# Kernel optimization log

Measured on AMD Instinct MI355X. Metric: run time of the kernel, lower is better.

The kernel has to match this reference:

```python
import jax, jax.numpy as jnp
import numpy as np

B, L, E, H = 64, 512, 128, 256


def setup_inputs() -> dict:
    key = jax.random.key(0)
    ks = jax.random.split(key, 16)
    s = 0.05
    return {
        "embedded_inputs": jax.random.normal(ks[0], (B, L, E), jnp.float32),
        "decoder_input": jax.random.normal(ks[1], (B, E), jnp.float32),
        "h0": jax.random.normal(ks[2], (B, H), jnp.float32),
        "c0": jax.random.normal(ks[3], (B, H), jnp.float32),
        "context": jax.random.normal(ks[4], (B, L, H), jnp.float32),
        # LSTM cell params
        "Wi": jax.random.normal(ks[5], (4 * H, E), jnp.float32) * s,
        "bi": jnp.zeros((4 * H,), jnp.float32),
        "Wh": jax.random.normal(ks[6], (4 * H, H), jnp.float32) * s,
        "bh": jnp.zeros((4 * H,), jnp.float32),
        # hidden_out: Linear(2H -> H)
        "Wo": jax.random.normal(ks[7], (H, 2 * H), jnp.float32) * s,
        "bo": jnp.zeros((H,), jnp.float32),
        # attention params: input_linear(H->H), context conv1d(H->H,k=1), V [H]
        "Wa_in": jax.random.normal(ks[8], (H, H), jnp.float32) * s,
        "ba_in": jnp.zeros((H,), jnp.float32),
        "Wa_ctx": jax.random.normal(ks[9], (H, H), jnp.float32) * s,
        "ba_ctx": jnp.zeros((H,), jnp.float32),
        "V": jax.random.normal(ks[10], (H,), jnp.float32) * s,
    }


def reference(embedded_inputs, decoder_input, h0, c0, context,
              Wi, bi, Wh, bh, Wo, bo, Wa_in, ba_in, Wa_ctx, ba_ctx, V):
    # Precompute projected context once (Conv1d with kernel 1 == per-position linear): [B,L,H]
    ctx_proj = jnp.einsum('blh,gh->blg', context, Wa_ctx) + ba_ctx

    def step(carry, _):
        dec_in, h, c, mask = carry
        gates = dec_in @ Wi.T + bi + h @ Wh.T + bh              # [B,4H]
        i_g, f_g, g_g, o_g = jnp.split(gates, 4, axis=1)
        i_g = jax.nn.sigmoid(i_g)
        f_g = jax.nn.sigmoid(f_g)
        g_g = jnp.tanh(g_g)
        o_g = jax.nn.sigmoid(o_g)
        c_t = f_g * c + i_g * g_g
        h_t = o_g * jnp.tanh(c_t)
        # attention
        inp = h_t @ Wa_in.T + ba_in                              # [B,H]
        scores = jnp.einsum('h,blh->bl', V, jnp.tanh(inp[:, None, :] + ctx_proj))
        scores = jnp.where(mask == 0, -jnp.inf, scores)
        alpha = jax.nn.softmax(scores, axis=1)                   # [B,L]
        att_hidden = jnp.einsum('bl,blh->bh', alpha, ctx_proj)
        hidden_t = jnp.tanh(jnp.concatenate([att_hidden, h_t], axis=1) @ Wo.T + bo)
        # pointer: argmax over still-available positions
        masked_outs = alpha * mask
        idx = jnp.argmax(masked_outs, axis=1)                    # [B]
        one_hot = jax.nn.one_hot(idx, L, dtype=mask.dtype)
        mask_next = mask * (1.0 - one_hot)
        dec_next = jnp.take_along_axis(embedded_inputs, idx[:, None, None], axis=1)[:, 0]
        return (dec_next, hidden_t, c_t, mask_next), (alpha, idx)

    mask0 = jnp.ones((B, L), jnp.float32)
    carry0 = (decoder_input, h0, c0, mask0)
    (dec_f, h_f, c_f, _), (alphas, ptrs) = jax.lax.scan(step, carry0, None, length=L)
    outputs = jnp.transpose(alphas, (1, 0, 2))                   # [B,L,L]
    pointers = jnp.transpose(ptrs, (1, 0))                       # [B,L]
    return outputs, pointers, h_f, c_f
```

## Files before the change

kernel.cpp:

```cpp
#include <hip/hip_runtime.h>
#include <math.h>

#define SCOPE __HIP_MEMORY_SCOPE_AGENT

constexpr int Bn = 64, Ln = 512, En = 128, Hn = 256, Tn = 512;
constexpr int NBLK = 256, NTHR = 512;
constexpr int CTX_LD = 260, XPAD = 384, UPAD = 520;

constexpr int OFF_CTX = 0;
constexpr int OFF_SCR = 128 * CTX_LD;
constexpr int OFF_INP = OFF_SCR + 4096;
constexpr int OFF_SS  = OFF_INP + 256;
constexpr int OFF_ES  = OFF_SS + 128;
constexpr int OFF_MK  = OFF_ES + 128;
constexpr int OFF_VS  = OFF_MK + 128;
constexpr int OFF_GS  = OFF_VS + 256;
constexpr int OFF_ST  = OFF_GS + 256;
constexpr int OFF_WR  = OFF_ST + 64;
constexpr int OFF_BA  = OFF_WR + 64;
constexpr int OFF_HTL = OFF_BA + 256;
constexpr int SMEM_FL = OFF_HTL + 64;

constexpr size_t PTR_OFF = (size_t)Bn * Ln * Ln;
constexpr size_t HF_OFF  = PTR_OFF + (size_t)Bn * Ln;
constexpr size_t CF_OFF  = HF_OFF + (size_t)Bn * Hn;

constexpr int GQ_HT    = 0;
constexpr int GQ_HID   = 1024;
constexpr int GQ_ATT   = 2048;
constexpr int GQ_STATS = 6144;
constexpr int GQ_INPP  = 6208;
constexpr int GQ_STRIDE = 6208 + 16384;

__device__ __forceinline__ float fast_tanh(float x) {
  const float e = __expf(2.0f * x);
  return 1.0f - __fdividef(2.0f, 1.0f + e);
}
__device__ __forceinline__ float sigmoidf_(float x) {
  return 1.0f / (1.0f + expf(-x));
}
__device__ __forceinline__ void llc_storef(float* p, float v) {
  __hip_atomic_store(p, v, __ATOMIC_RELAXED, SCOPE);
}
__device__ __forceinline__ float4 llc_ld4(const float* p) {
  float4 r;
  asm volatile("global_load_dwordx4 %0, %1, off sc0 sc1\n\ts_waitcnt vmcnt(0)"
               : "=&v"(r) : "v"(p) : "memory");
  return r;
}
__device__ __forceinline__ void llc_ld4x4(const float* p0, const float* p1,
                                          const float* p2, const float* p3,
                                          float4& a, float4& b, float4& c, float4& d) {
  asm volatile(
      "global_load_dwordx4 %0, %4, off sc0 sc1\n\t"
      "global_load_dwordx4 %1, %5, off sc0 sc1\n\t"
      "global_load_dwordx4 %2, %6, off sc0 sc1\n\t"
      "global_load_dwordx4 %3, %7, off sc0 sc1\n\t"
      "s_waitcnt vmcnt(0)"
      : "=&v"(a), "=&v"(b), "=&v"(c), "=&v"(d)
      : "v"(p0), "v"(p1), "v"(p2), "v"(p3) : "memory");
}
__device__ __forceinline__ void llc_ld5(const float* p0, const float* p1,
                                        const float* p2, const float* p3,
                                        const float* p4,
                                        float4& a, float4& b, float4& c,
                                        float4& d, float4& e) {
  asm volatile(
      "global_load_dwordx4 %0, %5, off sc0 sc1\n\t"
      "global_load_dwordx4 %1, %6, off sc0 sc1\n\t"
      "global_load_dwordx4 %2, %7, off sc0 sc1\n\t"
      "global_load_dwordx4 %3, %8, off sc0 sc1\n\t"
      "global_load_dwordx4 %4, %9, off sc0 sc1\n\t"
      "s_waitcnt vmcnt(0)"
      : "=&v"(a), "=&v"(b), "=&v"(c), "=&v"(d), "=&v"(e)
      : "v"(p0), "v"(p1), "v"(p2), "v"(p3), "v"(p4) : "memory");
}

__device__ __forceinline__ void group_barrier16(unsigned* flags_g, int j, unsigned tgt) {
  asm volatile("s_waitcnt vmcnt(0)" ::: "memory");
  __syncthreads();
  if (threadIdx.x == 0)
    __hip_atomic_store(&flags_g[j * 32], tgt, __ATOMIC_RELAXED, SCOPE);
  if (threadIdx.x < 16) {
    long spins = 0;
    while (__hip_atomic_load(&flags_g[threadIdx.x * 32], __ATOMIC_RELAXED, SCOPE) < tgt) {
      __builtin_amdgcn_s_sleep(1);
      if (++spins > 50000000L) __builtin_trap();
    }
  }
  __syncthreads();
  asm volatile("" ::: "memory");
}

#define DOT4(acc, w4, x4) \
  acc = fmaf((w4).x, (x4).x, fmaf((w4).y, (x4).y, fmaf((w4).z, (x4).z, fmaf((w4).w, (x4).w, (acc)))))

__global__ void __launch_bounds__(NTHR, 1)
decoder_main(const float* __restrict__ emb, const float* __restrict__ dec0,
             const float* __restrict__ h0,  const float* __restrict__ c0,
             const float* __restrict__ ctxg,const float* __restrict__ Wi,
             const float* __restrict__ bi,  const float* __restrict__ Wh,
             const float* __restrict__ bh,  const float* __restrict__ Wo,
             const float* __restrict__ bo,  const float* __restrict__ Wain,
             const float* __restrict__ bain,const float* __restrict__ Wactx,
             const float* __restrict__ bactx,const float* __restrict__ Vv,
             float* __restrict__ out, unsigned* __restrict__ flags,
             float* __restrict__ wsd)
{
  extern __shared__ float sm[];
  float* ctx    = sm + OFF_CTX;
  float* scr    = sm + OFF_SCR;
  float* x_s    = sm + OFF_SCR;
  float* inp_s  = sm + OFF_INP;
  float* s_s    = sm + OFF_SS;
  float* e_s    = sm + OFF_ES;
  float* mask_s = sm + OFF_MK;
  float* V_s    = sm + OFF_VS;
  float* gsum   = sm + OFF_GS;
  float* stats_s= sm + OFF_ST;
  float* wred   = sm + OFF_WR;
  float* bain_s = sm + OFF_BA;
  float* htl_s  = sm + OFF_HTL;
  int*   wredi  = (int*)wred;

  const int tid = threadIdx.x, bid = blockIdx.x;
  const int gq = bid >> 4, j = bid & 15;
  const int bbj = j >> 2, ck = j & 3;
  const int b_ctx = gq * 4 + bbj;
  const int l0 = ck * 128;

  const int team = tid >> 3, seg8 = tid & 7;
  const int gteam = team >> 4, hloc = team & 15;
  const int r_abs = gteam * 256 + j * 16 + hloc;
  const int g2 = tid >> 1, half = tid & 1;
  const int r16loc = tid >> 5, seg32 = tid & 31;
  const int r16 = j * 16 + r16loc;
  const int hq = tid & 63, lg = tid >> 6;

  unsigned* flags_g = flags + gq * (16 * 32);
  float* wsg = wsd + (size_t)gq * GQ_STRIDE;

  float4 wg4[12];
  #pragma unroll
  for (int k = 0; k < 4; ++k) wg4[k] = *(const float4*)&Wi[(size_t)r_abs * En + k * 32 + seg8 * 4];
  #pragma unroll
  for (int k = 0; k < 8; ++k) wg4[4 + k] = *(const float4*)&Wh[(size_t)r_abs * Hn + k * 32 + seg8 * 4];
  const float bias_g = bi[r_abs] + bh[r_abs];

  float4 wa4[2];
  #pragma unroll
  for (int k = 0; k < 2; ++k)
    wa4[k] = *(const float4*)&Wain[(size_t)g2 * Hn + j * 16 + half * 8 + k * 4];

  float4 wo4[4];
  #pragma unroll
  for (int k = 0; k < 4; ++k) wo4[k] = *(const float4*)&Wo[(size_t)r16 * (2 * Hn) + k * 128 + seg32 * 4];
  const float bo_r = bo[r16];

  float cst = 0.0f;
  if (tid < 64) cst = c0[(size_t)(gq * 4 + (tid >> 4)) * Hn + j * 16 + (tid & 15)];

  if (tid < 128) mask_s[tid] = 1.0f;
  if (tid < 256) { V_s[tid] = Vv[tid]; bain_s[tid] = bain[tid]; }

  {
    const int gc = tid & 31, lgi = tid >> 5;
    float acc[8][8];
    #pragma unroll
    for (int a2 = 0; a2 < 8; ++a2)
      #pragma unroll
      for (int b2 = 0; b2 < 8; ++b2) acc[a2][b2] = 0.0f;
    float* stg_c = scr;
    float* stg_w = scr + 1024;
    for (int kc = 0; kc < 32; ++kc) {
      __syncthreads();
      for (int i = tid; i < 1024; i += NTHR) {
        int k = i & 7, l = i >> 3;
        stg_c[k * 128 + l] = ctxg[((size_t)(b_ctx * Ln + l0 + l)) * Hn + kc * 8 + k];
      }
      for (int i = tid; i < 2048; i += NTHR) {
        int k = i & 7, gg = i >> 3;
        stg_w[k * 256 + gg] = Wactx[(size_t)gg * Hn + kc * 8 + k];
      }
      __syncthreads();
      #pragma unroll
      for (int kk = 0; kk < 8; ++kk) {
        float cl[8], wgt[8];
        #pragma unroll
        for (int jj = 0; jj < 8; ++jj) cl[jj] = stg_c[kk * 128 + lgi * 8 + jj];
        #pragma unroll
        for (int jj = 0; jj < 8; ++jj) wgt[jj] = stg_w[kk * 256 + gc * 8 + jj];
        #pragma unroll
        for (int li = 0; li < 8; ++li)
          #pragma unroll
          for (int gi = 0; gi < 8; ++gi)
            acc[li][gi] = fmaf(cl[li], wgt[gi], acc[li][gi]);
      }
    }
    __syncthreads();
    #pragma unroll
    for (int li = 0; li < 8; ++li)
      #pragma unroll
      for (int gi = 0; gi < 8; ++gi)
        ctx[(lgi * 8 + li) * CTX_LD + gc * 8 + gi] = acc[li][gi] + bactx[gc * 8 + gi];
  }
  __syncthreads();

  unsigned tgt = 1;
  int w0 = 0, w1 = 0, w2 = 0, w3 = 0;

  for (int t = 0; t < Tn; ++t) {
    {
      if (tid < 256) {
        const int bbx = tid >> 6, h4 = tid & 63;
        float4 v;
        if (t == 0) v = *(const float4*)&h0[(size_t)(gq * 4 + bbx) * Hn + h4 * 4];
        else        v = llc_ld4(wsg + GQ_HID + bbx * 256 + h4 * 4);
        *(float4*)&x_s[bbx * XPAD + 128 + h4 * 4] = v;
      } else if (tid < 384) {
        const int i2 = tid - 256, bbx = i2 >> 5, k4 = i2 & 31;
        const int gb = gq * 4 + bbx;
        float4 v;
        if (t == 0) v = *(const float4*)&dec0[(size_t)gb * En + k4 * 4];
        else {
          const int wsel = (bbx == 0) ? w0 : (bbx == 1) ? w1 : (bbx == 2) ? w2 : w3;
          v = *(const float4*)&emb[((size_t)gb * Ln + wsel) * En + k4 * 4];
        }
        *(float4*)&x_s[bbx * XPAD + k4 * 4] = v;
      }
      __syncthreads();
      #pragma unroll
      for (int bb = 0; bb < 4; ++bb) {
        float acc = 0.0f;
        #pragma unroll
        for (int k = 0; k < 12; ++k) {
          const float4 x4 = *(const float4*)&x_s[bb * XPAD + k * 32 + seg8 * 4];
          DOT4(acc, wg4[k], x4);
        }
        acc += __shfl_xor(acc, 1, 64);
        acc += __shfl_xor(acc, 2, 64);
        acc += __shfl_xor(acc, 4, 64);
        if (seg8 == 0) gsum[bb * 64 + team] = acc + bias_g;
      }
      __syncthreads();
      if (tid < 64) {
        const int bbx = tid >> 4, hx = tid & 15;
        const float iv = gsum[bbx * 64 + hx];
        const float fv = gsum[bbx * 64 + 16 + hx];
        const float gv = gsum[bbx * 64 + 32 + hx];
        const float ov = gsum[bbx * 64 + 48 + hx];
        const float cn = sigmoidf_(fv) * cst + sigmoidf_(iv) * tanhf(gv);
        const float htv = sigmoidf_(ov) * tanhf(cn);
        cst = cn;
        htl_s[bbx * 16 + hx] = htv;
        llc_storef(wsg + GQ_HT + bbx * 256 + j * 16 + hx, htv);
        if (t == Tn - 1) out[CF_OFF + (size_t)(gq * 4 + bbx) * Hn + j * 16 + hx] = cn;
      }
      __syncthreads();
      {
        float pac[4];
        #pragma unroll
        for (int bb = 0; bb < 4; ++bb) {
          float acc = 0.0f;
          #pragma unroll
          for (int k = 0; k < 2; ++k) {
            const float4 x4 = *(const float4*)&htl_s[bb * 16 + half * 8 + k * 4];
            DOT4(acc, wa4[k], x4);
          }
          pac[bb] = acc;
        }
        #pragma unroll
        for (int bb = 0; bb < 4; ++bb) {
          const float o = __shfl_xor(pac[bb], 1, 64);
          pac[bb] += o;
        }
        if (half == 0) {
          #pragma unroll
          for (int bb = 0; bb < 4; ++bb)
            llc_storef(wsg + GQ_INPP + bb * 4096 + g2 * 16 + j, pac[bb]);
        }
      }
    }
    group_barrier16(flags_g, j, tgt++);

    {
      if (tid < 256) {
        const float* ib = wsg + GQ_INPP + bbj * 4096 + tid * 16;
        float4 a0, a1, a2, a3;
        llc_ld4x4(ib, ib + 4, ib + 8, ib + 12, a0, a1, a2, a3);
        const float s01 = ((a0.x + a0.y) + (a0.z + a0.w)) + ((a1.x + a1.y) + (a1.z + a1.w));
        const float s23 = ((a2.x + a2.y) + (a2.z + a2.w)) + ((a3.x + a3.y) + (a3.z + a3.w));
        inp_s[tid] = s01 + s23 + bain_s[tid];
      }
      __syncthreads();
      const float4 in4 = *(const float4*)&inp_s[hq * 4];
      const float4 v4  = *(const float4*)&V_s[hq * 4];
      float4 c4[16];
      #pragma unroll
      for (int li = 0; li < 16; ++li)
        c4[li] = *(const float4*)&ctx[(lg * 16 + li) * CTX_LD + hq * 4];
      #pragma unroll
      for (int li = 0; li < 16; ++li) {
        float p;
        p = v4.x * fast_tanh(in4.x + c4[li].x);
        p = fmaf(v4.y, fast_tanh(in4.y + c4[li].y), p);
        p = fmaf(v4.z, fast_tanh(in4.z + c4[li].z), p);
        p = fmaf(v4.w, fast_tanh(in4.w + c4[li].w), p);
        p += __shfl_xor(p, 1, 64);
        p += __shfl_xor(p, 2, 64);
        p += __shfl_xor(p, 4, 64);
        p += __shfl_xor(p, 8, 64);
        p += __shfl_xor(p, 16, 64);
        p += __shfl_xor(p, 32, 64);
        if (hq == 0) {
          const int l = lg * 16 + li;
          s_s[l] = (mask_s[l] == 0.0f) ? -INFINITY : p;
        }
      }
      __syncthreads();
      if (tid < 128) {
        const float sv = s_s[tid];
        const float e = expf(sv);
        e_s[tid] = e;
        float ssum = e;
        #pragma unroll
        for (int m = 1; m < 64; m <<= 1) ssum += __shfl_xor(ssum, m, 64);
        float cv = sv; int ci = tid;
        #pragma unroll
        for (int m = 1; m < 64; m <<= 1) {
          const float ov = __shfl_xor(cv, m, 64);
          const int   oi = __shfl_xor(ci, m, 64);
          if (ov > cv || (ov == cv && oi < ci)) { cv = ov; ci = oi; }
        }
        if ((tid & 63) == 0) {
          wred[tid >> 6] = ssum;
          wred[4 + (tid >> 6)] = cv;
          wredi[8 + (tid >> 6)] = ci;
        }
      }
      __syncthreads();
      if (tid == 0) {
        const float S = wred[0] + wred[1];
        float bv = wred[4]; int bI = wredi[8];
        if (wred[5] > bv || (wred[5] == bv && wredi[9] < bI)) { bv = wred[5]; bI = wredi[9]; }
        float* stb = wsg + GQ_STATS + (bbj * 4 + ck) * 4;
        llc_storef(stb + 0, S);
        llc_storef(stb + 1, bv);
        llc_storef(stb + 2, (float)(l0 + bI));
      }
      {
        float p0 = 0, p1 = 0, p2 = 0, p3 = 0;
        #pragma unroll
        for (int li = 0; li < 16; ++li) {
          const float ev = e_s[lg * 16 + li];
          p0 = fmaf(ev, c4[li].x, p0);
          p1 = fmaf(ev, c4[li].y, p1);
          p2 = fmaf(ev, c4[li].z, p2);
          p3 = fmaf(ev, c4[li].w, p3);
        }
        *(float4*)&scr[lg * 256 + hq * 4] = make_float4(p0, p1, p2, p3);
      }
      __syncthreads();
      if (tid < 256) {
        float a = 0.0f;
        #pragma unroll
        for (int r2 = 0; r2 < 8; ++r2) a += scr[r2 * 256 + tid];
        llc_storef(wsg + GQ_ATT + (bbj * 4 + ck) * 256 + tid, a);
      }
    }
    group_barrier16(flags_g, j, tgt++);

    {
      float4 a0, a1, a2, a3, htv4;
      if (tid >= 256 && tid < 272) {
        const float4 st = llc_ld4(wsg + GQ_STATS + (tid - 256) * 4);
        *(float4*)&stats_s[(tid - 256) * 4] = st;
      }
      if (tid < 256) {
        const int bbx = tid >> 6, h4 = tid & 63;
        const float* ab = wsg + GQ_ATT + bbx * 1024 + h4 * 4;
        llc_ld5(ab, ab + 256, ab + 512, ab + 768, wsg + GQ_HT + tid * 4,
                a0, a1, a2, a3, htv4);
      }
      __syncthreads();
      float Sb[4]; int wq[4];
      #pragma unroll
      for (int bb = 0; bb < 4; ++bb) {
        Sb[bb] = ((stats_s[(bb * 4 + 0) * 4] + stats_s[(bb * 4 + 1) * 4])
                  + stats_s[(bb * 4 + 2) * 4]) + stats_s[(bb * 4 + 3) * 4];
        float bv = stats_s[(bb * 4 + 0) * 4 + 1];
        int bI = (int)stats_s[(bb * 4 + 0) * 4 + 2];
        #pragma unroll
        for (int c2 = 1; c2 < 4; ++c2) {
          const float v2 = stats_s[(bb * 4 + c2) * 4 + 1];
          const int i2 = (int)stats_s[(bb * 4 + c2) * 4 + 2];
          if (v2 > bv || (v2 == bv && i2 < bI)) { bv = v2; bI = i2; }
        }
        wq[bb] = bI;
      }
      const float Sown = (bbj == 0) ? Sb[0] : (bbj == 1) ? Sb[1] : (bbj == 2) ? Sb[2] : Sb[3];
      const int wown = (bbj == 0) ? wq[0] : (bbj == 1) ? wq[1] : (bbj == 2) ? wq[2] : wq[3];
      if (tid < 32) {
        const float4 e4 = *(const float4*)&e_s[tid * 4];
        *(float4*)&out[(size_t)b_ctx * Ln * Ln + (size_t)t * Ln + l0 + tid * 4] =
            make_float4(e4.x / Sown, e4.y / Sown, e4.z / Sown, e4.w / Sown);
      }
      if (tid == 0) {
        if (wown >= l0 && wown < l0 + 128) mask_s[wown - l0] = 0.0f;
        if (ck == 0) out[PTR_OFF + (size_t)b_ctx * Ln + t] = (float)wown;
      }
      if (tid < 256) {
        const int bbx = tid >> 6, h4 = tid & 63;
        const float Sx = (bbx == 0) ? Sb[0] : (bbx == 1) ? Sb[1] : (bbx == 2) ? Sb[2] : Sb[3];
        float4 u4;
        u4.x = (((a0.x + a1.x) + a2.x) + a3.x) / Sx;
        u4.y = (((a0.y + a1.y) + a2.y) + a3.y) / Sx;
        u4.z = (((a0.z + a1.z) + a2.z) + a3.z) / Sx;
        u4.w = (((a0.w + a1.w) + a2.w) + a3.w) / Sx;
        *(float4*)&scr[bbx * UPAD + h4 * 4] = u4;
        *(float4*)&scr[bbx * UPAD + 256 + h4 * 4] = htv4;
      }
      __syncthreads();
      #pragma unroll
      for (int bb = 0; bb < 4; ++bb) {
        float acc = 0.0f;
        #pragma unroll
        for (int k = 0; k < 4; ++k) {
          const float4 x4 = *(const float4*)&scr[bb * UPAD + k * 128 + seg32 * 4];
          DOT4(acc, wo4[k], x4);
        }
        acc += __shfl_xor(acc, 1, 64);
        acc += __shfl_xor(acc, 2, 64);
        acc += __shfl_xor(acc, 4, 64);
        acc += __shfl_xor(acc, 8, 64);
        acc += __shfl_xor(acc, 16, 64);
        if (seg32 == 0) {
          const float hv = tanhf(acc + bo_r);
          llc_storef(wsg + GQ_HID + bb * 256 + r16, hv);
          if (t == Tn - 1) out[HF_OFF + (size_t)(gq * 4 + bb) * Hn + r16] = hv;
        }
      }
      w0 = wq[0]; w1 = wq[1]; w2 = wq[2]; w3 = wq[3];
    }
    group_barrier16(flags_g, j, tgt++);
  }
}

extern "C" void kernel_launch(void* const* d_in, const int* in_sizes, int n_in,
                              void* d_out, int out_size, void* d_ws, size_t ws_size,
                              hipStream_t stream) {
  (void)in_sizes; (void)n_in; (void)out_size; (void)ws_size;
  (void)hipFuncSetAttribute(reinterpret_cast<const void*>(decoder_main),
                            hipFuncAttributeMaxDynamicSharedMemorySize, SMEM_FL * 4);
  (void)hipMemsetAsync(d_ws, 0, 32768, stream);

  const float* emb   = (const float*)d_in[0];
  const float* dec0  = (const float*)d_in[1];
  const float* h0    = (const float*)d_in[2];
  const float* c0    = (const float*)d_in[3];
  const float* ctxg  = (const float*)d_in[4];
  const float* Wi    = (const float*)d_in[5];
  const float* bi    = (const float*)d_in[6];
  const float* Wh    = (const float*)d_in[7];
  const float* bh    = (const float*)d_in[8];
  const float* Wo    = (const float*)d_in[9];
  const float* bo    = (const float*)d_in[10];
  const float* Wain  = (const float*)d_in[11];
  const float* bain  = (const float*)d_in[12];
  const float* Wactx = (const float*)d_in[13];
  const float* bactx = (const float*)d_in[14];
  const float* V     = (const float*)d_in[15];

  unsigned* flags = (unsigned*)d_ws;
  float* wsd = (float*)((char*)d_ws + 32768);

  decoder_main<<<NBLK, NTHR, SMEM_FL * 4, stream>>>(
      emb, dec0, h0, c0, ctxg, Wi, bi, Wh, bh, Wo, bo, Wain, bain, Wactx, bactx, V,
      (float*)d_out, flags, wsd);
}
```

Before: 11.49 ms.

## Split work across 512 blocks with 2 batches per 16-block group

Doubles the grid to 512 blocks so each 16-block group handles 2 batch rows instead of 4, with each block owning 64 context positions. Per-block shared memory, register arrays and per-step matvec work are halved, and launch bounds now allow 4 blocks per CU. The score reduction is rewritten as a transpose-style shuffle tree, and context values are reloaded from LDS rather than held in registers. In exchange there are twice as many groups doing barrier synchronisation and more partial stats to merge through the last-level cache.

```diff
diff --git a/kernel.cpp b/kernel.cpp
--- a/kernel.cpp
+++ b/kernel.cpp
@@ -4,33 +4,32 @@
 #define SCOPE __HIP_MEMORY_SCOPE_AGENT
 
 constexpr int Bn = 64, Ln = 512, En = 128, Hn = 256, Tn = 512;
-constexpr int NBLK = 256, NTHR = 512;
-constexpr int CTX_LD = 260, XPAD = 384, UPAD = 520;
+constexpr int NBLK = 512, NTHR = 512;
+constexpr int CTX_LD = 256, XPAD = 384, UPAD = 520;
 
 constexpr int OFF_CTX = 0;
-constexpr int OFF_SCR = 128 * CTX_LD;
-constexpr int OFF_INP = OFF_SCR + 4096;
+constexpr int OFF_SCR = 64 * CTX_LD;
+constexpr int OFF_INP = OFF_SCR + 2048;
 constexpr int OFF_SS  = OFF_INP + 256;
-constexpr int OFF_ES  = OFF_SS + 128;
-constexpr int OFF_MK  = OFF_ES + 128;
-constexpr int OFF_VS  = OFF_MK + 128;
+constexpr int OFF_ES  = OFF_SS + 64;
+constexpr int OFF_MK  = OFF_ES + 64;
+constexpr int OFF_VS  = OFF_MK + 64;
 constexpr int OFF_GS  = OFF_VS + 256;
-constexpr int OFF_ST  = OFF_GS + 256;
-constexpr int OFF_WR  = OFF_ST + 64;
-constexpr int OFF_BA  = OFF_WR + 64;
+constexpr int OFF_ST  = OFF_GS + 128;
+constexpr int OFF_BA  = OFF_ST + 64;
 constexpr int OFF_HTL = OFF_BA + 256;
-constexpr int SMEM_FL = OFF_HTL + 64;
+constexpr int SMEM_FL = OFF_HTL + 32;
 
 constexpr size_t PTR_OFF = (size_t)Bn * Ln * Ln;
 constexpr size_t HF_OFF  = PTR_OFF + (size_t)Bn * Ln;
 constexpr size_t CF_OFF  = HF_OFF + (size_t)Bn * Hn;
 
 constexpr int GQ_HT    = 0;
-constexpr int GQ_HID   = 1024;
-constexpr int GQ_ATT   = 2048;
-constexpr int GQ_STATS = 6144;
-constexpr int GQ_INPP  = 6208;
-constexpr int GQ_STRIDE = 6208 + 16384;
+constexpr int GQ_HID   = 512;
+constexpr int GQ_ATT   = 1024;
+constexpr int GQ_STATS = 5120;
+constexpr int GQ_INPP  = 5184;
+constexpr int GQ_STRIDE = 5184 + 8192;
 
 __device__ __forceinline__ float fast_tanh(float x) {
   const float e = __expf(2.0f * x);
@@ -95,7 +94,7 @@
 #define DOT4(acc, w4, x4) \
   acc = fmaf((w4).x, (x4).x, fmaf((w4).y, (x4).y, fmaf((w4).z, (x4).z, fmaf((w4).w, (x4).w, (acc)))))
 
-__global__ void __launch_bounds__(NTHR, 1)
+__global__ void __launch_bounds__(NTHR, 4)
 decoder_main(const float* __restrict__ emb, const float* __restrict__ dec0,
              const float* __restrict__ h0,  const float* __restrict__ c0,
              const float* __restrict__ ctxg,const float* __restrict__ Wi,
@@ -118,16 +117,14 @@
   float* V_s    = sm + OFF_VS;
   float* gsum   = sm + OFF_GS;
   float* stats_s= sm + OFF_ST;
-  float* wred   = sm + OFF_WR;
   float* bain_s = sm + OFF_BA;
   float* htl_s  = sm + OFF_HTL;
-  int*   wredi  = (int*)wred;
 
   const int tid = threadIdx.x, bid = blockIdx.x;
   const int gq = bid >> 4, j = bid & 15;
-  const int bbj = j >> 2, ck = j & 3;
-  const int b_ctx = gq * 4 + bbj;
-  const int l0 = ck * 128;
+  const int bbj = j >> 3, ck = j & 7;
+  const int b_ctx = gq * 2 + bbj;
+  const int l0 = ck * 64;
 
   const int team = tid >> 3, seg8 = tid & 7;
   const int gteam = team >> 4, hloc = team & 15;
@@ -158,40 +155,40 @@
   const float bo_r = bo[r16];
 
   float cst = 0.0f;
-  if (tid < 64) cst = c0[(size_t)(gq * 4 + (tid >> 4)) * Hn + j * 16 + (tid & 15)];
-
-  if (tid < 128) mask_s[tid] = 1.0f;
+  if (tid < 32) cst = c0[(size_t)(gq * 2 + (tid >> 4)) * Hn + j * 16 + (tid & 15)];
+
+  if (tid < 64) mask_s[tid] = 1.0f;
   if (tid < 256) { V_s[tid] = Vv[tid]; bain_s[tid] = bain[tid]; }
 
   {
     const int gc = tid & 31, lgi = tid >> 5;
-    float acc[8][8];
+    float acc[4][8];
     #pragma unroll
-    for (int a2 = 0; a2 < 8; ++a2)
+    for (int a2 = 0; a2 < 4; ++a2)
       #pragma unroll
       for (int b2 = 0; b2 < 8; ++b2) acc[a2][b2] = 0.0f;
     float* stg_c = scr;
-    float* stg_w = scr + 1024;
-    for (int kc = 0; kc < 32; ++kc) {
-      __syncthreads();
+    float* stg_w = scr + 256;
+    for (int kc = 0; kc < 64; ++kc) {
+      __syncthreads();
+      if (tid < 256) {
+        const int k = tid >> 6, l = tid & 63;
+        stg_c[k * 64 + l] = ctxg[((size_t)(b_ctx * Ln + l0 + l)) * Hn + kc * 4 + k];
+      }
       for (int i = tid; i < 1024; i += NTHR) {
-        int k = i & 7, l = i >> 3;
-        stg_c[k * 128 + l] = ctxg[((size_t)(b_ctx * Ln + l0 + l)) * Hn + kc * 8 + k];
-      }
-      for (int i = tid; i < 2048; i += NTHR) {
-        int k = i & 7, gg = i >> 3;
-        stg_w[k * 256 + gg] = Wactx[(size_t)gg * Hn + kc * 8 + k];
-      }
-      __syncthreads();
-      #pragma unroll
-      for (int kk = 0; kk < 8; ++kk) {
-        float cl[8], wgt[8];
-        #pragma unroll
-        for (int jj = 0; jj < 8; ++jj) cl[jj] = stg_c[kk * 128 + lgi * 8 + jj];
+        const int k = i >> 8, gg = i & 255;
+        stg_w[k * 256 + gg] = Wactx[(size_t)gg * Hn + kc * 4 + k];
+      }
+      __syncthreads();
+      #pragma unroll
+      for (int kk = 0; kk < 4; ++kk) {
+        float cl[4], wgt[8];
+        #pragma unroll
+        for (int jj = 0; jj < 4; ++jj) cl[jj] = stg_c[kk * 64 + lgi * 4 + jj];
         #pragma unroll
         for (int jj = 0; jj < 8; ++jj) wgt[jj] = stg_w[kk * 256 + gc * 8 + jj];
         #pragma unroll
-        for (int li = 0; li < 8; ++li)
+        for (int li = 0; li < 4; ++li)
           #pragma unroll
           for (int gi = 0; gi < 8; ++gi)
             acc[li][gi] = fmaf(cl[li], wgt[gi], acc[li][gi]);
@@ -199,38 +196,38 @@
     }
     __syncthreads();
     #pragma unroll
-    for (int li = 0; li < 8; ++li)
+    for (int li = 0; li < 4; ++li)
       #pragma unroll
       for (int gi = 0; gi < 8; ++gi)
-        ctx[(lgi * 8 + li) * CTX_LD + gc * 8 + gi] = acc[li][gi] + bactx[gc * 8 + gi];
+        ctx[(lgi * 4 + li) * CTX_LD + gc * 8 + gi] = acc[li][gi] + bactx[gc * 8 + gi];
   }
   __syncthreads();
 
   unsigned tgt = 1;
-  int w0 = 0, w1 = 0, w2 = 0, w3 = 0;
+  int w0 = 0, w1 = 0;
 
   for (int t = 0; t < Tn; ++t) {
     {
-      if (tid < 256) {
+      if (tid < 128) {
         const int bbx = tid >> 6, h4 = tid & 63;
         float4 v;
-        if (t == 0) v = *(const float4*)&h0[(size_t)(gq * 4 + bbx) * Hn + h4 * 4];
+        if (t == 0) v = *(const float4*)&h0[(size_t)(gq * 2 + bbx) * Hn + h4 * 4];
         else        v = llc_ld4(wsg + GQ_HID + bbx * 256 + h4 * 4);
         *(float4*)&x_s[bbx * XPAD + 128 + h4 * 4] = v;
-      } else if (tid < 384) {
-        const int i2 = tid - 256, bbx = i2 >> 5, k4 = i2 & 31;
-        const int gb = gq * 4 + bbx;
+      } else if (tid < 192) {
+        const int i2 = tid - 128, bbx = i2 >> 5, k4 = i2 & 31;
+        const int gb = gq * 2 + bbx;
         float4 v;
         if (t == 0) v = *(const float4*)&dec0[(size_t)gb * En + k4 * 4];
         else {
-          const int wsel = (bbx == 0) ? w0 : (bbx == 1) ? w1 : (bbx == 2) ? w2 : w3;
+          const int wsel = (bbx == 0) ? w0 : w1;
           v = *(const float4*)&emb[((size_t)gb * Ln + wsel) * En + k4 * 4];
         }
         *(float4*)&x_s[bbx * XPAD + k4 * 4] = v;
       }
       __syncthreads();
       #pragma unroll
-      for (int bb = 0; bb < 4; ++bb) {
+      for (int bb = 0; bb < 2; ++bb) {
         float acc = 0.0f;
         #pragma unroll
         for (int k = 0; k < 12; ++k) {
@@ -243,7 +240,7 @@
         if (seg8 == 0) gsum[bb * 64 + team] = acc + bias_g;
       }
       __syncthreads();
-      if (tid < 64) {
+      if (tid < 32) {
         const int bbx = tid >> 4, hx = tid & 15;
         const float iv = gsum[bbx * 64 + hx];
         const float fv = gsum[bbx * 64 + 16 + hx];
@@ -254,13 +251,13 @@
         cst = cn;
         htl_s[bbx * 16 + hx] = htv;
         llc_storef(wsg + GQ_HT + bbx * 256 + j * 16 + hx, htv);
-        if (t == Tn - 1) out[CF_OFF + (size_t)(gq * 4 + bbx) * Hn + j * 16 + hx] = cn;
+        if (t == Tn - 1) out[CF_OFF + (size_t)(gq * 2 + bbx) * Hn + j * 16 + hx] = cn;
       }
       __syncthreads();
       {
-        float pac[4];
-        #pragma unroll
-        for (int bb = 0; bb < 4; ++bb) {
+        float pac[2];
+        #pragma unroll
+        for (int bb = 0; bb < 2; ++bb) {
           float acc = 0.0f;
           #pragma unroll
           for (int k = 0; k < 2; ++k) {
@@ -269,15 +266,11 @@
           }
           pac[bb] = acc;
         }
-        #pragma unroll
-        for (int bb = 0; bb < 4; ++bb) {
-          const float o = __shfl_xor(pac[bb], 1, 64);
-          pac[bb] += o;
-        }
+        pac[0] += __shfl_xor(pac[0], 1, 64);
+        pac[1] += __shfl_xor(pac[1], 1, 64);
         if (half == 0) {
-          #pragma unroll
-          for (int bb = 0; bb < 4; ++bb)
-            llc_storef(wsg + GQ_INPP + bb * 4096 + g2 * 16 + j, pac[bb]);
+          llc_storef(wsg + GQ_INPP + g2 * 16 + j, pac[0]);
+          llc_storef(wsg + GQ_INPP + 4096 + g2 * 16 + j, pac[1]);
         }
       }
     }
@@ -293,32 +286,44 @@
         inp_s[tid] = s01 + s23 + bain_s[tid];
       }
       __syncthreads();
-      const float4 in4 = *(const float4*)&inp_s[hq * 4];
-      const float4 v4  = *(const float4*)&V_s[hq * 4];
-      float4 c4[16];
-      #pragma unroll
-      for (int li = 0; li < 16; ++li)
-        c4[li] = *(const float4*)&ctx[(lg * 16 + li) * CTX_LD + hq * 4];
-      #pragma unroll
-      for (int li = 0; li < 16; ++li) {
-        float p;
-        p = v4.x * fast_tanh(in4.x + c4[li].x);
-        p = fmaf(v4.y, fast_tanh(in4.y + c4[li].y), p);
-        p = fmaf(v4.z, fast_tanh(in4.z + c4[li].z), p);
-        p = fmaf(v4.w, fast_tanh(in4.w + c4[li].w), p);
-        p += __shfl_xor(p, 1, 64);
-        p += __shfl_xor(p, 2, 64);
-        p += __shfl_xor(p, 4, 64);
-        p += __shfl_xor(p, 8, 64);
-        p += __shfl_xor(p, 16, 64);
-        p += __shfl_xor(p, 32, 64);
-        if (hq == 0) {
-          const int l = lg * 16 + li;
-          s_s[l] = (mask_s[l] == 0.0f) ? -INFINITY : p;
-        }
-      }
-      __syncthreads();
-      if (tid < 128) {
+      {
+        const float4 in4 = *(const float4*)&inp_s[hq * 4];
+        const float4 v4  = *(const float4*)&V_s[hq * 4];
+        float p0, p1, p2, p3, p4, p5, p6, p7;
+        #define SCORE_P(dst, li)                                             \
+          {                                                                  \
+            const float4 c4 = *(const float4*)&ctx[(lg * 8 + (li)) * CTX_LD + hq * 4]; \
+            float p;                                                         \
+            p = v4.x * fast_tanh(in4.x + c4.x);                              \
+            p = fmaf(v4.y, fast_tanh(in4.y + c4.y), p);                      \
+            p = fmaf(v4.z, fast_tanh(in4.z + c4.z), p);                      \
+            p = fmaf(v4.w, fast_tanh(in4.w + c4.w), p);                      \
+            dst = p;                                                         \
+          }
+        SCORE_P(p0, 0) SCORE_P(p1, 1) SCORE_P(p2, 2) SCORE_P(p3, 3)
+        SCORE_P(p4, 4) SCORE_P(p5, 5) SCORE_P(p6, 6) SCORE_P(p7, 7)
+        #undef SCORE_P
+        const bool hi32 = (hq & 32) != 0;
+        float s, q0, q1, q2, q3, r0, r1, t0;
+        s = hi32 ? p0 : p4; s = __shfl_xor(s, 32, 64); q0 = (hi32 ? p4 : p0) + s;
+        s = hi32 ? p1 : p5; s = __shfl_xor(s, 32, 64); q1 = (hi32 ? p5 : p1) + s;
+        s = hi32 ? p2 : p6; s = __shfl_xor(s, 32, 64); q2 = (hi32 ? p6 : p2) + s;
+        s = hi32 ? p3 : p7; s = __shfl_xor(s, 32, 64); q3 = (hi32 ? p7 : p3) + s;
+        const bool hi16 = (hq & 16) != 0;
+        s = hi16 ? q0 : q2; s = __shfl_xor(s, 16, 64); r0 = (hi16 ? q2 : q0) + s;
+        s = hi16 ? q1 : q3; s = __shfl_xor(s, 16, 64); r1 = (hi16 ? q3 : q1) + s;
+        const bool hi8 = (hq & 8) != 0;
+        s = hi8 ? r0 : r1; s = __shfl_xor(s, 8, 64); t0 = (hi8 ? r1 : r0) + s;
+        t0 += __shfl_xor(t0, 4, 64);
+        t0 += __shfl_xor(t0, 2, 64);
+        t0 += __shfl_xor(t0, 1, 64);
+        if ((hq & 7) == 0) {
+          const int l = lg * 8 + ((hq >> 3) & 7);
+          s_s[l] = (mask_s[l] == 0.0f) ? -INFINITY : t0;
+        }
+      }
+      __syncthreads();
+      if (tid < 64) {
         const float sv = s_s[tid];
         const float e = expf(sv);
         e_s[tid] = e;
@@ -332,32 +337,26 @@
           const int   oi = __shfl_xor(ci, m, 64);
           if (ov > cv || (ov == cv && oi < ci)) { cv = ov; ci = oi; }
         }
-        if ((tid & 63) == 0) {
-          wred[tid >> 6] = ssum;
-          wred[4 + (tid >> 6)] = cv;
-          wredi[8 + (tid >> 6)] = ci;
-        }
-      }
-      __syncthreads();
-      if (tid == 0) {
-        const float S = wred[0] + wred[1];
-        float bv = wred[4]; int bI = wredi[8];
-        if (wred[5] > bv || (wred[5] == bv && wredi[9] < bI)) { bv = wred[5]; bI = wredi[9]; }
-        float* stb = wsg + GQ_STATS + (bbj * 4 + ck) * 4;
-        llc_storef(stb + 0, S);
-        llc_storef(stb + 1, bv);
-        llc_storef(stb + 2, (float)(l0 + bI));
-      }
+        if (tid == 0) {
+          float* stb = wsg + GQ_STATS + (bbj * 8 + ck) * 4;
+          llc_storef(stb + 0, ssum);
+          llc_storef(stb + 1, cv);
+          llc_storef(stb + 2, (float)(l0 + ci));
+        }
+      }
+      __syncthreads();
       {
         float p0 = 0, p1 = 0, p2 = 0, p3 = 0;
         #pragma unroll
-        for (int li = 0; li < 16; ++li) {
-          const float ev = e_s[lg * 16 + li];
-          p0 = fmaf(ev, c4[li].x, p0);
-          p1 = fmaf(ev, c4[li].y, p1);
-          p2 = fmaf(ev, c4[li].z, p2);
-          p3 = fmaf(ev, c4[li].w, p3);
-        }
+        for (int li = 0; li < 8; ++li) {
+          const float ev = e_s[lg * 8 + li];
+          const float4 c4 = *(const float4*)&ctx[(lg * 8 + li) * CTX_LD + hq * 4];
+          p0 = fmaf(ev, c4.x, p0);
+          p1 = fmaf(ev, c4.y, p1);
+          p2 = fmaf(ev, c4.z, p2);
+          p3 = fmaf(ev, c4.w, p3);
+        }
+        __syncthreads();
         *(float4*)&scr[lg * 256 + hq * 4] = make_float4(p0, p1, p2, p3);
       }
       __syncthreads();
@@ -365,64 +364,72 @@
         float a = 0.0f;
         #pragma unroll
         for (int r2 = 0; r2 < 8; ++r2) a += scr[r2 * 256 + tid];
-        llc_storef(wsg + GQ_ATT + (bbj * 4 + ck) * 256 + tid, a);
+        llc_storef(wsg + GQ_ATT + (bbj * 8 + ck) * 256 + tid, a);
       }
     }
     group_barrier16(flags_g, j, tgt++);
 
     {
-      float4 a0, a1, a2, a3, htv4;
+      float4 sum4 = make_float4(0, 0, 0, 0), htv4 = make_float4(0, 0, 0, 0);
       if (tid >= 256 && tid < 272) {
         const float4 st = llc_ld4(wsg + GQ_STATS + (tid - 256) * 4);
         *(float4*)&stats_s[(tid - 256) * 4] = st;
       }
-      if (tid < 256) {
+      if (tid < 128) {
         const int bbx = tid >> 6, h4 = tid & 63;
-        const float* ab = wsg + GQ_ATT + bbx * 1024 + h4 * 4;
-        llc_ld5(ab, ab + 256, ab + 512, ab + 768, wsg + GQ_HT + tid * 4,
-                a0, a1, a2, a3, htv4);
-      }
-      __syncthreads();
-      float Sb[4]; int wq[4];
-      #pragma unroll
-      for (int bb = 0; bb < 4; ++bb) {
-        Sb[bb] = ((stats_s[(bb * 4 + 0) * 4] + stats_s[(bb * 4 + 1) * 4])
-                  + stats_s[(bb * 4 + 2) * 4]) + stats_s[(bb * 4 + 3) * 4];
-        float bv = stats_s[(bb * 4 + 0) * 4 + 1];
-        int bI = (int)stats_s[(bb * 4 + 0) * 4 + 2];
-        #pragma unroll
-        for (int c2 = 1; c2 < 4; ++c2) {
-          const float v2 = stats_s[(bb * 4 + c2) * 4 + 1];
-          const int i2 = (int)stats_s[(bb * 4 + c2) * 4 + 2];
+        const float* ab = wsg + GQ_ATT + bbx * 2048 + h4 * 4;
+        float4 a0, a1, a2, a3, b0, b1, b2, b3;
+        llc_ld4x4(ab, ab + 256, ab + 512, ab + 768, a0, a1, a2, a3);
+        sum4.x = ((a0.x + a1.x) + (a2.x + a3.x));
+        sum4.y = ((a0.y + a1.y) + (a2.y + a3.y));
+        sum4.z = ((a0.z + a1.z) + (a2.z + a3.z));
+        sum4.w = ((a0.w + a1.w) + (a2.w + a3.w));
+        llc_ld5(ab + 1024, ab + 1280, ab + 1536, ab + 1792,
+                wsg + GQ_HT + bbx * 256 + h4 * 4, b0, b1, b2, b3, htv4);
+        sum4.x += ((b0.x + b1.x) + (b2.x + b3.x));
+        sum4.y += ((b0.y + b1.y) + (b2.y + b3.y));
+        sum4.z += ((b0.z + b1.z) + (b2.z + b3.z));
+        sum4.w += ((b0.w + b1.w) + (b2.w + b3.w));
+      }
+      __syncthreads();
+      float Sb[2]; int wq[2];
+      #pragma unroll
+      for (int bb = 0; bb < 2; ++bb) {
+        float Ssum = 0.0f;
+        #pragma unroll
+        for (int c2 = 0; c2 < 8; ++c2) Ssum += stats_s[(bb * 8 + c2) * 4];
+        Sb[bb] = Ssum;
+        float bv = stats_s[(bb * 8 + 0) * 4 + 1];
+        int bI = (int)stats_s[(bb * 8 + 0) * 4 + 2];
+        #pragma unroll
+        for (int c2 = 1; c2 < 8; ++c2) {
+          const float v2 = stats_s[(bb * 8 + c2) * 4 + 1];
+          const int i2 = (int)stats_s[(bb * 8 + c2) * 4 + 2];
           if (v2 > bv || (v2 == bv && i2 < bI)) { bv = v2; bI = i2; }
         }
         wq[bb] = bI;
       }
-      const float Sown = (bbj == 0) ? Sb[0] : (bbj == 1) ? Sb[1] : (bbj == 2) ? Sb[2] : Sb[3];
-      const int wown = (bbj == 0) ? wq[0] : (bbj == 1) ? wq[1] : (bbj == 2) ? wq[2] : wq[3];
-      if (tid < 32) {
+      const float Sown = (bbj == 0) ? Sb[0] : Sb[1];
+      const int wown = (bbj == 0) ? wq[0] : wq[1];
+      if (tid < 16) {
         const float4 e4 = *(const float4*)&e_s[tid * 4];
         *(float4*)&out[(size_t)b_ctx * Ln * Ln + (size_t)t * Ln + l0 + tid * 4] =
             make_float4(e4.x / Sown, e4.y / Sown, e4.z / Sown, e4.w / Sown);
       }
       if (tid == 0) {
-        if (wown >= l0 && wown < l0 + 128) mask_s[wown - l0] = 0.0f;
+        if (wown >= l0 && wown < l0 + 64) mask_s[wown - l0] = 0.0f;
         if (ck == 0) out[PTR_OFF + (size_t)b_ctx * Ln + t] = (float)wown;
       }
-      if (tid < 256) {
+      if (tid < 128) {
         const int bbx = tid >> 6, h4 = tid & 63;
-        const float Sx = (bbx == 0) ? Sb[0] : (bbx == 1) ? Sb[1] : (bbx == 2) ? Sb[2] : Sb[3];
-        float4 u4;
-        u4.x = (((a0.x + a1.x) + a2.x) + a3.x) / Sx;
-        u4.y = (((a0.y + a1.y) + a2.y) + a3.y) / Sx;
-        u4.z = (((a0.z + a1.z) + a2.z) + a3.z) / Sx;
-        u4.w = (((a0.w + a1.w) + a2.w) + a3.w) / Sx;
-        *(float4*)&scr[bbx * UPAD + h4 * 4] = u4;
+        const float Sx = (bbx == 0) ? Sb[0] : Sb[1];
+        *(float4*)&scr[bbx * UPAD + h4 * 4] =
+            make_float4(sum4.x / Sx, sum4.y / Sx, sum4.z / Sx, sum4.w / Sx);
         *(float4*)&scr[bbx * UPAD + 256 + h4 * 4] = htv4;
       }
       __syncthreads();
       #pragma unroll
-      for (int bb = 0; bb < 4; ++bb) {
+      for (int bb = 0; bb < 2; ++bb) {
         float acc = 0.0f;
         #pragma unroll
         for (int k = 0; k < 4; ++k) {
@@ -437,10 +444,10 @@
         if (seg32 == 0) {
           const float hv = tanhf(acc + bo_r);
           llc_storef(wsg + GQ_HID + bb * 256 + r16, hv);
-          if (t == Tn - 1) out[HF_OFF + (size_t)(gq * 4 + bb) * Hn + r16] = hv;
-        }
-      }
-      w0 = wq[0]; w1 = wq[1]; w2 = wq[2]; w3 = wq[3];
+          if (t == Tn - 1) out[HF_OFF + (size_t)(gq * 2 + bb) * Hn + r16] = hv;
+        }
+      }
+      w0 = wq[0]; w1 = wq[1];
     }
     group_barrier16(flags_g, j, tgt++);
   }
@@ -452,7 +459,7 @@
   (void)in_sizes; (void)n_in; (void)out_size; (void)ws_size;
   (void)hipFuncSetAttribute(reinterpret_cast<const void*>(decoder_main),
                             hipFuncAttributeMaxDynamicSharedMemorySize, SMEM_FL * 4);
-  (void)hipMemsetAsync(d_ws, 0, 32768, stream);
+  (void)hipMemsetAsync(d_ws, 0, 65536, stream);
 
   const float* emb   = (const float*)d_in[0];
   const float* dec0  = (const float*)d_in[1];
@@ -472,7 +479,7 @@
   const float* V     = (const float*)d_in[15];
 
   unsigned* flags = (unsigned*)d_ws;
-  float* wsd = (float*)((char*)d_ws + 32768);
+  float* wsd = (float*)((char*)d_ws + 65536);
 
   decoder_main<<<NBLK, NTHR, SMEM_FL * 4, stream>>>(
       emb, dec0, h0, c0, ctxg, Wi, bi, Wh, bh, Wo, bo, Wain, bain, Wactx, bactx, V,
```

Result: slower. 14.54 ms (+26.6%).
